# Optimization experiments

Measured on AMD Instinct MI355X. Metric: run time of the kernel, lower is better.

Reference implementation:

```python
import math
import jax, jax.numpy as jnp
import numpy as np

D_MODEL = 256
N_HEADS = 4
HEAD_DIM = D_MODEL // N_HEADS
MAX_REL = 30


def _rel_pos_encodings(t, d_model):
    # sinusoidal table over clipped relative distances -> [t, t, d_model]
    n = 2 * MAX_REL + 1
    positions = jnp.arange(n, dtype=jnp.float32)[:, None]
    div_term = jnp.exp(jnp.arange(0, d_model, 2, dtype=jnp.float32) * (-math.log(10000.0) / d_model))
    ang = positions * div_term                      # [n, d/2]
    enc = jnp.stack([jnp.sin(ang), jnp.cos(ang)], axis=-1).reshape(n, d_model)
    rng = jnp.arange(t)
    final_mat = jnp.clip(rng[None, :] - rng[:, None], -MAX_REL, MAX_REL) + MAX_REL  # [t, t]
    return enc[final_mat]                           # [t, t, d_model]


def setup_inputs() -> dict:
    key = jax.random.key(0)
    ks = jax.random.split(key, 12)
    d = D_MODEL
    s = 1.0 / math.sqrt(d)
    inp = {
        "inputs": jax.random.normal(ks[0], (16, 512, d), dtype=jnp.float32),
        "ln_gamma": jnp.ones((d,), jnp.float32),
        "ln_beta": jnp.zeros((d,), jnp.float32),
        "Wq": jax.random.normal(ks[1], (d, d), jnp.float32) * s,
        "bq": jnp.zeros((d,), jnp.float32),
        "Wk": jax.random.normal(ks[2], (d, d), jnp.float32) * s,
        "bk": jnp.zeros((d,), jnp.float32),
        "Wv": jax.random.normal(ks[3], (d, d), jnp.float32) * s,
        "bv": jnp.zeros((d,), jnp.float32),
        "Wpos": jax.random.normal(ks[4], (d, d), jnp.float32) * s,
        "bpos": jnp.zeros((d,), jnp.float32),
        "Wo": jax.random.normal(ks[5], (d, d), jnp.float32) * s,
        "bo": jnp.zeros((d,), jnp.float32),
        "u_bias": jax.random.normal(ks[6], (1, N_HEADS, 1, HEAD_DIM), jnp.float32) * 0.02,
        "v_bias": jax.random.normal(ks[7], (1, N_HEADS, 1, HEAD_DIM), jnp.float32) * 0.02,
    }
    return inp


def reference(inputs, ln_gamma, ln_beta, Wq, bq, Wk, bk, Wv, bv, Wpos, bpos, Wo, bo, u_bias, v_bias):
    b, t, d = inputs.shape
    h, hd = N_HEADS, HEAD_DIM
    # LayerNorm (eps=1e-5, torch default)
    mu = jnp.mean(inputs, axis=-1, keepdims=True)
    var = jnp.mean(jnp.square(inputs - mu), axis=-1, keepdims=True)
    x = (inputs - mu) * jax.lax.rsqrt(var + 1e-5) * ln_gamma + ln_beta

    def split_heads(y):
        return y.reshape(b, t, h, hd).transpose(0, 2, 1, 3)  # b h t d

    q = split_heads(x @ Wq.T + bq)
    k = split_heads(x @ Wk.T + bk)
    v = split_heads(x @ Wv.T + bv)

    rel = jax.lax.stop_gradient(_rel_pos_encodings(t, d))    # [t, t, d]
    pos = (rel @ Wpos.T + bpos).reshape(t, t, h, hd)         # [t1, t2, h, hd]

    qk_score = jnp.einsum('bhtd,bhsd->bhts', q + u_bias, k)
    pos_score = jnp.einsum('bhtd,tshd->bhts', q + v_bias, pos)
    scores = (qk_score + pos_score) / math.sqrt(hd)
    attn = jax.nn.softmax(scores, axis=-1)
    ctx = jnp.einsum('bhts,bhsd->bhtd', attn, v)
    ctx = ctx.transpose(0, 2, 1, 3).reshape(b, t, d)
    return ctx @ Wo.T + bo
```

## Files before the change

kernel.cpp:

```cpp
#include <hip/hip_runtime.h>
#include <hip/hip_bf16.h>
#include <math.h>

#define B 16
#define T 512
#define D 256
#define H 4
#define HD 64
#define MAXREL 30
#define NREL 61
#define M_ROWS (B*T)
#define QBLK 128

typedef __attribute__((ext_vector_type(8))) short bf16x8;
typedef __attribute__((ext_vector_type(4))) float f32x4;
typedef unsigned short ush;

__device__ inline ush f2b(float f) {
    __hip_bfloat16 h = __float2bfloat16(f);
    union { __hip_bfloat16 h; ush u; } c; c.h = h; return c.u;
}
__device__ inline float b2f(ush u) {
    union { ush u; __hip_bfloat16 h; } c; c.u = u; return __bfloat162float(c.h);
}
__device__ inline unsigned int pk2(float a, float b) {
    __hip_bfloat162 h = __float22bfloat162_rn(make_float2(a, b));
    union { __hip_bfloat162 h; unsigned int u; } c; c.h = h; return c.u;
}
__device__ inline int swz(int row, int byteoff) {
    return row * 128 + (byteoff ^ ((row & 7) << 4));
}
__device__ inline int swz256(int row, int byteoff) {
    return row * 256 + (byteoff ^ ((row & 7) << 4));
}
__device__ inline int swz512(int row, int byteoff) {
    return row * 512 + (byteoff ^ ((row & 7) << 4));
}

#define SCL 0.1803368801111204f

__global__ __launch_bounds__(256) void prep_kernel(const float* __restrict__ x,
                                                   const float* __restrict__ gamma,
                                                   const float* __restrict__ beta,
                                                   ush* __restrict__ xb,
                                                   const float* __restrict__ Wq, const float* __restrict__ Wk,
                                                   const float* __restrict__ Wv, const float* __restrict__ Wo,
                                                   ush* __restrict__ wb,
                                                   const float* __restrict__ Wpos,
                                                   const float* __restrict__ bpos,
                                                   ush* __restrict__ pospb) {
    __shared__ __attribute__((aligned(16))) ush wpS[64 * 256];
    int bid = blockIdx.x;
    int tid = threadIdx.x;
    if (bid < 512) {
        int lane = tid & 63;
        float4 g = *(const float4*)(gamma + lane * 4);
        float4 bb = *(const float4*)(beta + lane * 4);
        #pragma unroll
        for (int it = 0; it < 4; ++it) {
            int row = bid * 16 + it * 4 + (tid >> 6);
            const float* xr = x + (size_t)row * D;
            float4 v = *(const float4*)(xr + lane * 4);
            float s = v.x + v.y + v.z + v.w;
            #pragma unroll
            for (int off = 32; off; off >>= 1) s += __shfl_xor(s, off);
            float mu = s * (1.f / 256.f);
            float dx = v.x - mu, dy = v.y - mu, dz = v.z - mu, dw = v.w - mu;
            float vs = dx*dx + dy*dy + dz*dz + dw*dw;
            #pragma unroll
            for (int off = 32; off; off >>= 1) vs += __shfl_xor(vs, off);
            float rstd = rsqrtf(vs * (1.f / 256.f) + 1e-5f);
            ushort4 o;
            o.x = f2b(dx * rstd * g.x + bb.x);
            o.y = f2b(dy * rstd * g.y + bb.y);
            o.z = f2b(dz * rstd * g.z + bb.z);
            o.w = f2b(dw * rstd * g.w + bb.w);
            *(ushort4*)(xb + (size_t)row * D + lane * 4) = o;
        }
    } else if (bid < 512 + 256) {
        int b2 = bid - 512;
        int z = b2 >> 6, xblk = b2 & 63;
        const float* src = z == 0 ? Wq : z == 1 ? Wk : z == 2 ? Wv : Wo;
        int idx = (xblk * 256 + tid) * 4;
        float4 v = *(const float4*)(src + idx);
        ushort4 o;
        o.x = f2b(v.x); o.y = f2b(v.y); o.z = f2b(v.z); o.w = f2b(v.w);
        *(ushort4*)(wb + (size_t)z * 65536 + idx) = o;
    } else {
        int h = bid - 768;
        int w = tid >> 6, l = tid & 63, lg = l >> 4, ln = l & 15;
        const float* wsrc = Wpos + (size_t)(h * 64) * D;
        #pragma unroll
        for (int c = 0; c < 16; ++c) {
            int idx = c * 256 + tid;
            int row = idx >> 6, col = (idx & 63) * 4;
            float4 v = *(const float4*)(wsrc + (size_t)row * D + col);
            ushort4 o; o.x = f2b(v.x); o.y = f2b(v.y); o.z = f2b(v.z); o.w = f2b(v.w);
            *(ushort4*)((char*)wpS + swz512(row, col * 2)) = o;
        }
        int p = w * 16 + ln;
        bf16x8 af[8];
        #pragma unroll
        for (int ks = 0; ks < 8; ++ks) {
            #pragma unroll
            for (int j = 0; j < 8; ++j) {
                int k = ks * 32 + lg * 8 + j;
                int i = k >> 1;
                float dt = __expf(-(2.f * i) * (9.210340371976184f / 256.f));
                float ang = (float)p * dt;
                float v = (k & 1) ? __cosf(ang) : __sinf(ang);
                af[ks][j] = (short)f2b(v);
            }
        }
        __syncthreads();
        f32x4 acc[4] = {};
        #pragma unroll
        for (int ks = 0; ks < 8; ++ks) {
            int kbyte = (ks * 32 + lg * 8) * 2;
            #pragma unroll
            for (int ct = 0; ct < 4; ++ct) {
                bf16x8 bf = *(const bf16x8*)((const char*)wpS + swz512(ct * 16 + ln, kbyte));
                acc[ct] = __builtin_amdgcn_mfma_f32_16x16x32_bf16(af[ks], bf, acc[ct], 0, 0, 0);
            }
        }
        #pragma unroll
        for (int ct = 0; ct < 4; ++ct) {
            int dcol = ct * 16 + ln;
            float bb = bpos[h * 64 + dcol];
            #pragma unroll
            for (int r = 0; r < 4; ++r) {
                int pr = w * 16 + lg * 4 + r;
                pospb[(size_t)h * 4096 + pr * 64 + dcol] = f2b(acc[ct][r] + bb);
            }
        }
    }
}

__global__ __launch_bounds__(256, 3) void qkv_mfma(const ush* __restrict__ A,
                                                   const ush* __restrict__ wball,
                                                   const float* __restrict__ bq,
                                                   const float* __restrict__ bk,
                                                   const float* __restrict__ bv,
                                                   ush* __restrict__ qb,
                                                   ush* __restrict__ kbuf,
                                                   ush* __restrict__ vtb) {
    __shared__ __attribute__((aligned(16))) ush A_s[128 * 128];
    __shared__ __attribute__((aligned(16))) ush B_s[64 * 128];
    int tid = threadIdx.x;
    int w = tid >> 6, l = tid & 63;
    int lg = l >> 4, ln = l & 15;
    int wr = w >> 1, wc = w & 1;
    int i0 = blockIdx.x * 128;
    int j0 = blockIdx.y * 64;
    int z = blockIdx.z;
    const ush* Wp = wball + (size_t)z * 65536 + (size_t)j0 * D;
    const ush* Ap = A + (size_t)i0 * D;
    const float* bias = z == 0 ? bq : (z == 1 ? bk : bv);
    f32x4 acc[2][4] = {};

    #pragma unroll 1
    for (int kb2 = 0; kb2 < 2; ++kb2) {
        int k0 = kb2 * 128;
        if (kb2) __syncthreads();
        #pragma unroll
        for (int c = 0; c < 8; ++c) {
            int u = c * 256 + tid;
            int row = u >> 4, sub = u & 15;
            *(bf16x8*)((char*)A_s + swz256(row, sub * 16)) = *(const bf16x8*)(Ap + (size_t)row * D + k0 + sub * 8);
        }
        #pragma unroll
        for (int c = 0; c < 4; ++c) {
            int u = c * 256 + tid;
            int row = u >> 4, sub = u & 15;
            *(bf16x8*)((char*)B_s + swz256(row, sub * 16)) = *(const bf16x8*)(Wp + (size_t)row * D + k0 + sub * 8);
        }
        __syncthreads();
        __builtin_amdgcn_s_setprio(1);
        #pragma unroll
        for (int ksub = 0; ksub < 4; ++ksub) {
            int kbyte = ksub * 64 + lg * 16;
            bf16x8 af[2], bfr[4];
            #pragma unroll
            for (int mi = 0; mi < 2; ++mi)
                af[mi] = *(const bf16x8*)((const char*)B_s + swz256(wr * 32 + mi * 16 + ln, kbyte));
            #pragma unroll
            for (int ni = 0; ni < 4; ++ni)
                bfr[ni] = *(const bf16x8*)((const char*)A_s + swz256(wc * 64 + ni * 16 + ln, kbyte));
            #pragma unroll
            for (int mi = 0; mi < 2; ++mi)
                #pragma unroll
                for (int ni = 0; ni < 4; ++ni)
                    acc[mi][ni] = __builtin_amdgcn_mfma_f32_16x16x32_bf16(af[mi], bfr[ni], acc[mi][ni], 0, 0, 0);
        }
        __builtin_amdgcn_s_setprio(0);
    }

    if (z == 2) {
        #pragma unroll
        for (int mi = 0; mi < 2; ++mi) {
            int jb = j0 + wr * 32 + mi * 16 + lg * 4;
            float4 bv4 = *(const float4*)(bias + jb);
            float bvv[4] = {bv4.x, bv4.y, bv4.z, bv4.w};
            #pragma unroll
            for (int ni = 0; ni < 4; ++ni) {
                int t = i0 + wc * 64 + ni * 16 + ln;
                #pragma unroll
                for (int r = 0; r < 4; ++r)
                    vtb[(size_t)(jb + r) * M_ROWS + t] = f2b(acc[mi][ni][r] + bvv[r]);
            }
        }
    } else {
        ush* ob = (z == 0) ? qb : kbuf;
        #pragma unroll
        for (int mi = 0; mi < 2; ++mi) {
            int jb = j0 + wr * 32 + mi * 16 + lg * 4;
            float4 bv4 = *(const float4*)(bias + jb);
            #pragma unroll
            for (int ni = 0; ni < 4; ++ni) {
                int t = i0 + wc * 64 + ni * 16 + ln;
                ushort4 o;
                o.x = f2b(acc[mi][ni][0] + bv4.x); o.y = f2b(acc[mi][ni][1] + bv4.y);
                o.z = f2b(acc[mi][ni][2] + bv4.z); o.w = f2b(acc[mi][ni][3] + bv4.w);
                *(ushort4*)(ob + (size_t)t * D + jb) = o;
            }
        }
    }
}

__global__ __launch_bounds__(256, 2) void outproj_mfma(const ush* __restrict__ A,
                                                       const ush* __restrict__ W,
                                                       const float* __restrict__ bias,
                                                       float* __restrict__ of) {
    __shared__ __attribute__((aligned(16))) ush A_s[64 * 128];
    __shared__ __attribute__((aligned(16))) ush B_s[64 * 128];
    int tid = threadIdx.x;
    int w = tid >> 6, l = tid & 63;
    int lg = l >> 4, ln = l & 15;
    int wr = w >> 1, wc = w & 1;
    int i0 = blockIdx.x * 64;
    int j0 = blockIdx.y * 64;
    const ush* Ap = A + (size_t)i0 * D;
    const ush* Wp = W + (size_t)j0 * D;
    f32x4 acc[2][2] = {};

    #pragma unroll 1
    for (int kb2 = 0; kb2 < 2; ++kb2) {
        int k0 = kb2 * 128;
        if (kb2) __syncthreads();
        #pragma unroll
        for (int c = 0; c < 4; ++c) {
            int u = c * 256 + tid;
            int row = u >> 4, sub = u & 15;
            *(bf16x8*)((char*)A_s + swz256(row, sub * 16)) = *(const bf16x8*)(Ap + (size_t)row * D + k0 + sub * 8);
            *(bf16x8*)((char*)B_s + swz256(row, sub * 16)) = *(const bf16x8*)(Wp + (size_t)row * D + k0 + sub * 8);
        }
        __syncthreads();
        __builtin_amdgcn_s_setprio(1);
        #pragma unroll
        for (int ksub = 0; ksub < 4; ++ksub) {
            int kbyte = ksub * 64 + lg * 16;
            bf16x8 af[2], bfr[2];
            #pragma unroll
            for (int mi = 0; mi < 2; ++mi)
                af[mi] = *(const bf16x8*)((const char*)B_s + swz256(wr * 32 + mi * 16 + ln, kbyte));
            #pragma unroll
            for (int ni = 0; ni < 2; ++ni)
                bfr[ni] = *(const bf16x8*)((const char*)A_s + swz256(wc * 32 + ni * 16 + ln, kbyte));
            #pragma unroll
            for (int mi = 0; mi < 2; ++mi)
                #pragma unroll
                for (int ni = 0; ni < 2; ++ni)
                    acc[mi][ni] = __builtin_amdgcn_mfma_f32_16x16x32_bf16(af[mi], bfr[ni], acc[mi][ni], 0, 0, 0);
        }
        __builtin_amdgcn_s_setprio(0);
    }

    #pragma unroll
    for (int mi = 0; mi < 2; ++mi) {
        int jb = j0 + wr * 32 + mi * 16 + lg * 4;
        float4 bv4 = *(const float4*)(bias + jb);
        #pragma unroll
        for (int ni = 0; ni < 2; ++ni) {
            int t = i0 + wc * 32 + ni * 16 + ln;
            float4 o;
            o.x = acc[mi][ni][0] + bv4.x; o.y = acc[mi][ni][1] + bv4.y;
            o.z = acc[mi][ni][2] + bv4.z; o.w = acc[mi][ni][3] + bv4.w;
            *(float4*)(of + (size_t)t * D + jb) = o;
        }
    }
}

__global__ __launch_bounds__(512, 2) void attn_mfma(const ush* __restrict__ qb,
                                                    const ush* __restrict__ kb,
                                                    const ush* __restrict__ vtb,
                                                    const ush* __restrict__ pospb,
                                                    const float* __restrict__ u_bias,
                                                    const float* __restrict__ v_bias,
                                                    ush* __restrict__ ctxb) {
    __shared__ __attribute__((aligned(16))) ush Kd[2][64 * 64];
    __shared__ __attribute__((aligned(16))) ush Vd[2][64 * 64];
    __shared__ __attribute__((aligned(16))) ush pdS[8][16 * 66];
    __shared__ __attribute__((aligned(16))) ush PlS[8][16 * 64];

    int tid = threadIdx.x;
    int w = tid >> 6;
    int l = tid & 63;
    int lg = l >> 4, ln = l & 15;
    int bh = blockIdx.x;
    int b = bh >> 2, h = bh & 3;
    int t0 = blockIdx.y * QBLK;
    const size_t baseBH = ((size_t)b * T) * D + h * HD;

    bf16x8 qu[2], qv[2];
    {
        const ush* qrow = qb + baseBH + (size_t)(t0 + w * 16 + ln) * D;
        int c0 = lg * 8;
        #pragma unroll
        for (int ks = 0; ks < 2; ++ks) {
            bf16x8 ld = *(const bf16x8*)(qrow + ks * 32 + c0);
            float4 ub0 = *(const float4*)(u_bias + h * HD + ks * 32 + c0);
            float4 ub1 = *(const float4*)(u_bias + h * HD + ks * 32 + c0 + 4);
            float4 vb0 = *(const float4*)(v_bias + h * HD + ks * 32 + c0);
            float4 vb1 = *(const float4*)(v_bias + h * HD + ks * 32 + c0 + 4);
            float ubv[8] = {ub0.x,ub0.y,ub0.z,ub0.w,ub1.x,ub1.y,ub1.z,ub1.w};
            float vbv[8] = {vb0.x,vb0.y,vb0.z,vb0.w,vb1.x,vb1.y,vb1.z,vb1.w};
            #pragma unroll
            for (int j = 0; j < 8; ++j) {
                float f = b2f((ush)ld[j]);
                qu[ks][j] = (short)f2b((f + ubv[j]) * SCL);
                qv[ks][j] = (short)f2b((f + vbv[j]) * SCL);
            }
        }
    }

    int r0 = tid >> 3, c0 = tid & 7;
    const ush* kbase = kb + baseBH;
    const ush* vbase = vtb + (size_t)(h * HD) * M_ROWS + (size_t)b * T;
    const ush* pbase = pospb + (size_t)h * 4096;

    {
        bf16x8 pp0 = *(const bf16x8*)(pbase + r0 * 64 + c0 * 8);
        bf16x8 k0 = *(const bf16x8*)(kbase + (size_t)r0 * D + c0 * 8);
        bf16x8 v0 = *(const bf16x8*)(vbase + (size_t)r0 * M_ROWS + c0 * 8);
        *(bf16x8*)((char*)Kd[1] + swz(r0, c0 * 16)) = pp0;
        *(bf16x8*)((char*)Kd[0] + swz(r0, c0 * 16)) = k0;
        *(bf16x8*)((char*)Vd[0] + swz(r0, c0 * 16)) = v0;
    }
    bf16x8 sk0 = *(const bf16x8*)(kbase + (size_t)(64 + r0) * D + c0 * 8);
    bf16x8 sv0 = *(const bf16x8*)(vbase + (size_t)r0 * M_ROWS + 64 + c0 * 8);
    __syncthreads();

    ush* pdW = pdS[w];
    {
        f32x4 pacc[4] = {};
        #pragma unroll
        for (int ks = 0; ks < 2; ++ks)
            #pragma unroll
            for (int ct = 0; ct < 4; ++ct) {
                bf16x8 bf = *(const bf16x8*)((const char*)Kd[1] + swz(ct * 16 + ln, (ks * 32 + lg * 8) * 2));
                pacc[ct] = __builtin_amdgcn_mfma_f32_16x16x32_bf16(qv[ks], bf, pacc[ct], 0, 0, 0);
            }
        #pragma unroll
        for (int ct = 0; ct < 4; ++ct)
            #pragma unroll
            for (int r = 0; r < 4; ++r)
                pdW[(lg * 4 + r) * 66 + ct * 16 + ln] = f2b(pacc[ct][r]);
    }
    float pdlo = b2f(pdW[ln * 66 + 0]);
    float pdhi = b2f(pdW[ln * 66 + 60]);
    __syncthreads();

    f32x4 lacc = {};
    f32x4 o_acc[4] = {};
    ush* pw = PlS[w];
    bf16x8 ones;
    #pragma unroll
    for (int j = 0; j < 8; ++j) ones[j] = (short)0x3F80;
    int cur = 0;

    for (int st = 0; st < 8; ++st) {
        int s0 = st * 64;
        if (st < 7) {
            *(bf16x8*)((char*)Kd[cur ^ 1] + swz(r0, c0 * 16)) = sk0;
            *(bf16x8*)((char*)Vd[cur ^ 1] + swz(r0, c0 * 16)) = sv0;
        }
        if (st < 6) {
            int sn = s0 + 128;
            sk0 = *(const bf16x8*)(kbase + (size_t)(sn + r0) * D + c0 * 8);
            sv0 = *(const bf16x8*)(vbase + (size_t)r0 * M_ROWS + sn + c0 * 8);
        }

        const char* Kc = (const char*)Kd[cur];
        const char* Vc = (const char*)Vd[cur];

        int dlt = s0 - t0;
        int below = dlt <= -(QBLK + MAXREL + 33);
        (void)below;
        float cinit;
        f32x4 sacc[4];
        if (dlt >= 192) cinit = pdhi;
        else if (dlt <= -128) cinit = pdlo;
        else cinit = 0.f;
        #pragma unroll
        for (int ct = 0; ct < 4; ++ct)
            #pragma unroll
            for (int r = 0; r < 4; ++r) sacc[ct][r] = cinit;

        __builtin_amdgcn_s_setprio(1);
        #pragma unroll
        for (int ks = 0; ks < 2; ++ks)
            #pragma unroll
            for (int ct = 0; ct < 4; ++ct) {
                bf16x8 kf = *(const bf16x8*)(Kc + swz(ct * 16 + ln, (ks * 32 + lg * 8) * 2));
                sacc[ct] = __builtin_amdgcn_mfma_f32_16x16x32_bf16(kf, qu[ks], sacc[ct], 0, 0, 0);
            }
        __builtin_amdgcn_s_setprio(0);

        if (dlt > -128 && dlt < 192) {
            int t_glob = t0 + w * 16 + ln;
            #pragma unroll
            for (int ct = 0; ct < 4; ++ct) {
                #pragma unroll
                for (int r = 0; r < 4; ++r) {
                    int s_g = s0 + ct * 16 + lg * 4 + r;
                    int rel = s_g - t_glob;
                    rel = rel < -MAXREL ? -MAXREL : (rel > MAXREL ? MAXREL : rel);
                    sacc[ct][r] += b2f(pdW[ln * 66 + rel + MAXREL]);
                }
            }
        }

        #pragma unroll
        for (int ct = 0; ct < 4; ++ct)
            #pragma unroll
            for (int r = 0; r < 4; ++r)
                sacc[ct][r] = exp2f(sacc[ct][r]);

        #pragma unroll
        for (int ct = 0; ct < 4; ++ct)
            #pragma unroll
            for (int rr = 0; rr < 2; ++rr)
                *(unsigned int*)((char*)pw + swz(ln, (ct * 16 + lg * 4 + rr * 2) * 2)) =
                    pk2(sacc[ct][rr * 2], sacc[ct][rr * 2 + 1]);

        __builtin_amdgcn_s_setprio(1);
        #pragma unroll
        for (int ks = 0; ks < 2; ++ks) {
            bf16x8 pa = *(const bf16x8*)((const char*)pw + swz(ln, (ks * 32 + lg * 8) * 2));
            #pragma unroll
            for (int cd = 0; cd < 4; ++cd) {
                bf16x8 bv8 = *(const bf16x8*)(Vc + swz(cd * 16 + ln, (ks * 32 + lg * 8) * 2));
                o_acc[cd] = __builtin_amdgcn_mfma_f32_16x16x32_bf16(pa, bv8, o_acc[cd], 0, 0, 0);
            }
            lacc = __builtin_amdgcn_mfma_f32_16x16x32_bf16(pa, ones, lacc, 0, 0, 0);
        }
        __builtin_amdgcn_s_setprio(0);

        __syncthreads();
        cur ^= 1;
    }

    float inv[4];
    #pragma unroll
    for (int r = 0; r < 4; ++r) inv[r] = 1.f / lacc[r];
    #pragma unroll
    for (int cd = 0; cd < 4; ++cd)
        #pragma unroll
        for (int r = 0; r < 4; ++r) {
            int t_loc = w * 16 + lg * 4 + r;
            ctxb[baseBH + (size_t)(t0 + t_loc) * D + cd * 16 + ln] = f2b(o_acc[cd][r] * inv[r]);
        }
}

extern "C" void kernel_launch(void* const* d_in, const int* in_sizes, int n_in,
                              void* d_out, int out_size, void* d_ws, size_t ws_size,
                              hipStream_t stream) {
    const float* inputs  = (const float*)d_in[0];
    const float* ln_g    = (const float*)d_in[1];
    const float* ln_b    = (const float*)d_in[2];
    const float* Wq      = (const float*)d_in[3];
    const float* bq      = (const float*)d_in[4];
    const float* Wk      = (const float*)d_in[5];
    const float* bk      = (const float*)d_in[6];
    const float* Wv      = (const float*)d_in[7];
    const float* bv      = (const float*)d_in[8];
    const float* Wpos    = (const float*)d_in[9];
    const float* bpos    = (const float*)d_in[10];
    const float* Wo      = (const float*)d_in[11];
    const float* bo      = (const float*)d_in[12];
    const float* u_bias  = (const float*)d_in[13];
    const float* v_bias  = (const float*)d_in[14];
    float* out = (float*)d_out;

    char* w = (char*)d_ws;
    ush* xb    = (ush*)w;  w += (size_t)M_ROWS * D * 2;
    ush* qb    = (ush*)w;  w += (size_t)M_ROWS * D * 2;
    ush* kbuf  = (ush*)w;  w += (size_t)M_ROWS * D * 2;
    ush* vtb   = (ush*)w;  w += (size_t)M_ROWS * D * 2;
    ush* ctxb  = (ush*)w;  w += (size_t)M_ROWS * D * 2;
    ush* wb    = (ush*)w;  w += (size_t)4 * 65536 * 2;
    ush* pospb = (ush*)w;  w += (size_t)4 * 64 * 64 * 2;

    prep_kernel<<<512 + 256 + 4, 256, 0, stream>>>(inputs, ln_g, ln_b, xb,
                                                   Wq, Wk, Wv, Wo, wb,
                                                   Wpos, bpos, pospb);

    qkv_mfma<<<dim3(M_ROWS / 128, 4, 3), 256, 0, stream>>>(xb, wb, bq, bk, bv, qb, kbuf, vtb);

    attn_mfma<<<dim3(B * H, T / QBLK), 512, 0, stream>>>(qb, kbuf, vtb, pospb, u_bias, v_bias, ctxb);

    outproj_mfma<<<dim3(M_ROWS / 64, 4), 256, 0, stream>>>(ctxb, wb + 3 * 65536, bo, out);
}
```

Measured before the change: 41.19 us.

## Fuse LayerNorm and weight conversion into QKV GEMM, drop prep kernel

Removes the separate prep kernel. LayerNorm is now computed inside the QKV GEMM while it loads its A tiles, and fp32 weights are converted to bf16 on the fly in both the QKV and out-projection GEMMs. The Wpos projection runs as extra z-slice blocks of the fused launch, and most of those blocks exit immediately. This saves one launch and the bf16 xb round-trip through global memory. In exchange, each QKV block recomputes LayerNorm statistics for its rows (12x redundant across y and z), reads fp32 inputs twice, reconverts weights in every block, and computes variance with the E[x²]-mu² form.

```diff
diff --git a/kernel.cpp b/kernel.cpp
--- a/kernel.cpp
+++ b/kernel.cpp
@@ -39,55 +39,30 @@
 
 #define SCL 0.1803368801111204f
 
-__global__ __launch_bounds__(256) void prep_kernel(const float* __restrict__ x,
-                                                   const float* __restrict__ gamma,
-                                                   const float* __restrict__ beta,
-                                                   ush* __restrict__ xb,
-                                                   const float* __restrict__ Wq, const float* __restrict__ Wk,
-                                                   const float* __restrict__ Wv, const float* __restrict__ Wo,
-                                                   ush* __restrict__ wb,
-                                                   const float* __restrict__ Wpos,
-                                                   const float* __restrict__ bpos,
-                                                   ush* __restrict__ pospb) {
-    __shared__ __attribute__((aligned(16))) ush wpS[64 * 256];
-    int bid = blockIdx.x;
+__global__ __launch_bounds__(256, 3) void qkvp_fused(const float* __restrict__ x,
+                                                     const float* __restrict__ gamma,
+                                                     const float* __restrict__ beta,
+                                                     const float* __restrict__ Wq,
+                                                     const float* __restrict__ Wk,
+                                                     const float* __restrict__ Wv,
+                                                     const float* __restrict__ Wpos,
+                                                     const float* __restrict__ bpos,
+                                                     ush* __restrict__ pospb,
+                                                     const float* __restrict__ bq,
+                                                     const float* __restrict__ bk,
+                                                     const float* __restrict__ bv,
+                                                     ush* __restrict__ qb,
+                                                     ush* __restrict__ kbuf,
+                                                     ush* __restrict__ vtb) {
+    __shared__ __attribute__((aligned(16))) char pool[128 * 256 + 64 * 256];
+    ush* A_s = (ush*)pool;
+    ush* B_s = (ush*)(pool + 32768);
     int tid = threadIdx.x;
-    if (bid < 512) {
-        int lane = tid & 63;
-        float4 g = *(const float4*)(gamma + lane * 4);
-        float4 bb = *(const float4*)(beta + lane * 4);
-        #pragma unroll
-        for (int it = 0; it < 4; ++it) {
-            int row = bid * 16 + it * 4 + (tid >> 6);
-            const float* xr = x + (size_t)row * D;
-            float4 v = *(const float4*)(xr + lane * 4);
-            float s = v.x + v.y + v.z + v.w;
-            #pragma unroll
-            for (int off = 32; off; off >>= 1) s += __shfl_xor(s, off);
-            float mu = s * (1.f / 256.f);
-            float dx = v.x - mu, dy = v.y - mu, dz = v.z - mu, dw = v.w - mu;
-            float vs = dx*dx + dy*dy + dz*dz + dw*dw;
-            #pragma unroll
-            for (int off = 32; off; off >>= 1) vs += __shfl_xor(vs, off);
-            float rstd = rsqrtf(vs * (1.f / 256.f) + 1e-5f);
-            ushort4 o;
-            o.x = f2b(dx * rstd * g.x + bb.x);
-            o.y = f2b(dy * rstd * g.y + bb.y);
-            o.z = f2b(dz * rstd * g.z + bb.z);
-            o.w = f2b(dw * rstd * g.w + bb.w);
-            *(ushort4*)(xb + (size_t)row * D + lane * 4) = o;
-        }
-    } else if (bid < 512 + 256) {
-        int b2 = bid - 512;
-        int z = b2 >> 6, xblk = b2 & 63;
-        const float* src = z == 0 ? Wq : z == 1 ? Wk : z == 2 ? Wv : Wo;
-        int idx = (xblk * 256 + tid) * 4;
-        float4 v = *(const float4*)(src + idx);
-        ushort4 o;
-        o.x = f2b(v.x); o.y = f2b(v.y); o.z = f2b(v.z); o.w = f2b(v.w);
-        *(ushort4*)(wb + (size_t)z * 65536 + idx) = o;
-    } else {
-        int h = bid - 768;
+
+    if (blockIdx.z == 3) {
+        if (blockIdx.x != 0) return;
+        ush* wpS = (ush*)pool;
+        int h = blockIdx.y;
         int w = tid >> 6, l = tid & 63, lg = l >> 4, ln = l & 15;
         const float* wsrc = Wpos + (size_t)(h * 64) * D;
         #pragma unroll
@@ -133,46 +108,71 @@
                 pospb[(size_t)h * 4096 + pr * 64 + dcol] = f2b(acc[ct][r] + bb);
             }
         }
-    }
-}
-
-__global__ __launch_bounds__(256, 3) void qkv_mfma(const ush* __restrict__ A,
-                                                   const ush* __restrict__ wball,
-                                                   const float* __restrict__ bq,
-                                                   const float* __restrict__ bk,
-                                                   const float* __restrict__ bv,
-                                                   ush* __restrict__ qb,
-                                                   ush* __restrict__ kbuf,
-                                                   ush* __restrict__ vtb) {
-    __shared__ __attribute__((aligned(16))) ush A_s[128 * 128];
-    __shared__ __attribute__((aligned(16))) ush B_s[64 * 128];
-    int tid = threadIdx.x;
+        return;
+    }
+
     int w = tid >> 6, l = tid & 63;
     int lg = l >> 4, ln = l & 15;
     int wr = w >> 1, wc = w & 1;
     int i0 = blockIdx.x * 128;
     int j0 = blockIdx.y * 64;
     int z = blockIdx.z;
-    const ush* Wp = wball + (size_t)z * 65536 + (size_t)j0 * D;
-    const ush* Ap = A + (size_t)i0 * D;
+    const float* W = z == 0 ? Wq : (z == 1 ? Wk : Wv);
     const float* bias = z == 0 ? bq : (z == 1 ? bk : bv);
+
+    int lrow = tid >> 1, half = tid & 1;
+    const float* xr = x + (size_t)(i0 + lrow) * D + half * 128;
+    float s = 0.f, ss = 0.f;
+    #pragma unroll 8
+    for (int c = 0; c < 32; ++c) {
+        float4 v = *(const float4*)(xr + c * 4);
+        s += v.x + v.y + v.z + v.w;
+        ss += v.x * v.x + v.y * v.y + v.z * v.z + v.w * v.w;
+    }
+    s += __shfl_xor(s, 1);
+    ss += __shfl_xor(ss, 1);
+    float mu = s * (1.f / 256.f);
+    float rstd = rsqrtf(ss * (1.f / 256.f) - mu * mu + 1e-5f);
+
     f32x4 acc[2][4] = {};
 
     #pragma unroll 1
     for (int kb2 = 0; kb2 < 2; ++kb2) {
         int k0 = kb2 * 128;
         if (kb2) __syncthreads();
-        #pragma unroll
-        for (int c = 0; c < 8; ++c) {
-            int u = c * 256 + tid;
-            int row = u >> 4, sub = u & 15;
-            *(bf16x8*)((char*)A_s + swz256(row, sub * 16)) = *(const bf16x8*)(Ap + (size_t)row * D + k0 + sub * 8);
+        if (half == kb2) {
+            #pragma unroll
+            for (int c = 0; c < 16; ++c) {
+                float4 a0 = *(const float4*)(xr + c * 8);
+                float4 a1 = *(const float4*)(xr + c * 8 + 4);
+                const float* gc = gamma + half * 128 + c * 8;
+                const float* bc = beta + half * 128 + c * 8;
+                float4 g0 = *(const float4*)(gc), g1 = *(const float4*)(gc + 4);
+                float4 b0 = *(const float4*)(bc), b1 = *(const float4*)(bc + 4);
+                bf16x8 o;
+                o[0] = (short)f2b((a0.x - mu) * rstd * g0.x + b0.x);
+                o[1] = (short)f2b((a0.y - mu) * rstd * g0.y + b0.y);
+                o[2] = (short)f2b((a0.z - mu) * rstd * g0.z + b0.z);
+                o[3] = (short)f2b((a0.w - mu) * rstd * g0.w + b0.w);
+                o[4] = (short)f2b((a1.x - mu) * rstd * g1.x + b1.x);
+                o[5] = (short)f2b((a1.y - mu) * rstd * g1.y + b1.y);
+                o[6] = (short)f2b((a1.z - mu) * rstd * g1.z + b1.z);
+                o[7] = (short)f2b((a1.w - mu) * rstd * g1.w + b1.w);
+                *(bf16x8*)((char*)A_s + swz256(lrow, c * 16)) = o;
+            }
         }
         #pragma unroll
         for (int c = 0; c < 4; ++c) {
-            int u = c * 256 + tid;
-            int row = u >> 4, sub = u & 15;
-            *(bf16x8*)((char*)B_s + swz256(row, sub * 16)) = *(const bf16x8*)(Wp + (size_t)row * D + k0 + sub * 8);
+            int e = c * 256 + tid;
+            int rw = e >> 4, sub = e & 15;
+            const float* wsrc = W + (size_t)(j0 + rw) * D + k0 + sub * 8;
+            float4 w0 = *(const float4*)(wsrc), w1 = *(const float4*)(wsrc + 4);
+            bf16x8 o;
+            o[0] = (short)f2b(w0.x); o[1] = (short)f2b(w0.y);
+            o[2] = (short)f2b(w0.z); o[3] = (short)f2b(w0.w);
+            o[4] = (short)f2b(w1.x); o[5] = (short)f2b(w1.y);
+            o[6] = (short)f2b(w1.z); o[7] = (short)f2b(w1.w);
+            *(bf16x8*)((char*)B_s + swz256(rw, sub * 16)) = o;
         }
         __syncthreads();
         __builtin_amdgcn_s_setprio(1);
@@ -228,7 +228,7 @@
 }
 
 __global__ __launch_bounds__(256, 2) void outproj_mfma(const ush* __restrict__ A,
-                                                       const ush* __restrict__ W,
+                                                       const float* __restrict__ W,
                                                        const float* __restrict__ bias,
                                                        float* __restrict__ of) {
     __shared__ __attribute__((aligned(16))) ush A_s[64 * 128];
@@ -240,7 +240,6 @@
     int i0 = blockIdx.x * 64;
     int j0 = blockIdx.y * 64;
     const ush* Ap = A + (size_t)i0 * D;
-    const ush* Wp = W + (size_t)j0 * D;
     f32x4 acc[2][2] = {};
 
     #pragma unroll 1
@@ -252,7 +251,14 @@
             int u = c * 256 + tid;
             int row = u >> 4, sub = u & 15;
             *(bf16x8*)((char*)A_s + swz256(row, sub * 16)) = *(const bf16x8*)(Ap + (size_t)row * D + k0 + sub * 8);
-            *(bf16x8*)((char*)B_s + swz256(row, sub * 16)) = *(const bf16x8*)(Wp + (size_t)row * D + k0 + sub * 8);
+            const float* wsrc = W + (size_t)(j0 + row) * D + k0 + sub * 8;
+            float4 w0 = *(const float4*)(wsrc), w1 = *(const float4*)(wsrc + 4);
+            bf16x8 o;
+            o[0] = (short)f2b(w0.x); o[1] = (short)f2b(w0.y);
+            o[2] = (short)f2b(w0.z); o[3] = (short)f2b(w0.w);
+            o[4] = (short)f2b(w1.x); o[5] = (short)f2b(w1.y);
+            o[6] = (short)f2b(w1.z); o[7] = (short)f2b(w1.w);
+            *(bf16x8*)((char*)B_s + swz256(row, sub * 16)) = o;
         }
         __syncthreads();
         __builtin_amdgcn_s_setprio(1);
@@ -394,13 +400,11 @@
         const char* Vc = (const char*)Vd[cur];
 
         int dlt = s0 - t0;
-        int below = dlt <= -(QBLK + MAXREL + 33);
-        (void)below;
         float cinit;
-        f32x4 sacc[4];
         if (dlt >= 192) cinit = pdhi;
         else if (dlt <= -128) cinit = pdlo;
         else cinit = 0.f;
+        f32x4 sacc[4];
         #pragma unroll
         for (int ct = 0; ct < 4; ++ct)
             #pragma unroll
@@ -493,21 +497,17 @@
     float* out = (float*)d_out;
 
     char* w = (char*)d_ws;
-    ush* xb    = (ush*)w;  w += (size_t)M_ROWS * D * 2;
     ush* qb    = (ush*)w;  w += (size_t)M_ROWS * D * 2;
     ush* kbuf  = (ush*)w;  w += (size_t)M_ROWS * D * 2;
     ush* vtb   = (ush*)w;  w += (size_t)M_ROWS * D * 2;
     ush* ctxb  = (ush*)w;  w += (size_t)M_ROWS * D * 2;
-    ush* wb    = (ush*)w;  w += (size_t)4 * 65536 * 2;
     ush* pospb = (ush*)w;  w += (size_t)4 * 64 * 64 * 2;
 
-    prep_kernel<<<512 + 256 + 4, 256, 0, stream>>>(inputs, ln_g, ln_b, xb,
-                                                   Wq, Wk, Wv, Wo, wb,
-                                                   Wpos, bpos, pospb);
-
-    qkv_mfma<<<dim3(M_ROWS / 128, 4, 3), 256, 0, stream>>>(xb, wb, bq, bk, bv, qb, kbuf, vtb);
+    qkvp_fused<<<dim3(M_ROWS / 128, 4, 4), 256, 0, stream>>>(inputs, ln_g, ln_b,
+                                                             Wq, Wk, Wv, Wpos, bpos, pospb,
+                                                             bq, bk, bv, qb, kbuf, vtb);
 
     attn_mfma<<<dim3(B * H, T / QBLK), 512, 0, stream>>>(qb, kbuf, vtb, pospb, u_bias, v_bias, ctxb);
 
-    outproj_mfma<<<dim3(M_ROWS / 64, 4), 256, 0, stream>>>(ctxb, wb + 3 * 65536, bo, out);
-}
+    outproj_mfma<<<dim3(M_ROWS / 64, 4), 256, 0, stream>>>(ctxb, Wo, bo, out);
+}
```

Result: slower. 67.25 us (+63.3%).
